# Performance work log

Hardware: AMD Instinct MI355X
Metric: run time of the kernel (lower is better)

Reference implementation:

```python
import jax, jax.numpy as jnp
import numpy as np

N_NODES = 50000
NEG_SLOPE = 0.2  # PyG GATConv default leaky_relu slope


def _segment_softmax(alpha, dst, num_segments):
    # numerically stable softmax over edges grouped by destination node
    m = jax.ops.segment_max(alpha, dst, num_segments=num_segments)
    e = jnp.exp(alpha - m[dst])
    s = jax.ops.segment_sum(e, dst, num_segments=num_segments)
    return e / (s[dst] + 1e-16)


def _gat_conv(h, src, dst, edge_attr, W, We, att_src, att_dst, att_edge, b, num_nodes):
    # h: [N, F_in] -> [N, C] with heads=1, concat=True, add_self_loops=False
    hs = h @ W                          # [N, C]
    ea = edge_attr @ We                 # [E, C]
    a_src = hs @ att_src                # [N]
    a_dst = hs @ att_dst                # [N]
    a_edge = ea @ att_edge              # [E]
    alpha = a_src[src] + a_dst[dst] + a_edge
    alpha = jax.nn.leaky_relu(alpha, NEG_SLOPE)
    alpha = _segment_softmax(alpha, dst, num_nodes)
    msg = hs[src] * alpha[:, None]      # [E, C]
    out = jax.ops.segment_sum(msg, dst, num_segments=num_nodes)
    return out + b


def setup_inputs() -> dict:
    key = jax.random.key(0)
    ks = jax.random.split(key, 16)
    N, E = N_NODES, 500000
    num_authors, a_dim, sbert, c1, c2 = 50000, 128, 384, 32, 128

    def glorot(k, shape):
        lim = float(np.sqrt(6.0 / (shape[0] + shape[-1])))
        return jax.random.uniform(k, shape, jnp.float32, -lim, lim)

    return {
        "x": jnp.arange(N, dtype=jnp.int64) % num_authors,
        "edge_index": jax.random.randint(ks[0], (2, E), 0, N, dtype=jnp.int64),
        "edge_attr": jax.random.normal(ks[1], (E, sbert), jnp.float32),
        "emb": jax.random.normal(ks[2], (num_authors, a_dim), jnp.float32),
        "W1": glorot(ks[3], (a_dim, c1)),
        "We1": glorot(ks[4], (sbert, c1)),
        "att_src1": glorot(ks[5], (c1,)),
        "att_dst1": glorot(ks[6], (c1,)),
        "att_edge1": glorot(ks[7], (c1,)),
        "b1": jnp.zeros((c1,), jnp.float32),
        "W2": glorot(ks[8], (c1, c2)),
        "We2": glorot(ks[9], (sbert, c2)),
        "att_src2": glorot(ks[10], (c2,)),
        "att_dst2": glorot(ks[11], (c2,)),
        "att_edge2": glorot(ks[12], (c2,)),
        "b2": jnp.zeros((c2,), jnp.float32),
    }


def reference(x, edge_index, edge_attr, emb, W1, We1, att_src1, att_dst1, att_edge1, b1,
              W2, We2, att_src2, att_dst2, att_edge2, b2):
    src, dst = edge_index[0], edge_index[1]
    h = emb[x]  # author embedding lookup [N, 128]
    h = _gat_conv(h, src, dst, edge_attr, W1, We1, att_src1, att_dst1, att_edge1, b1, N_NODES)
    h = jax.nn.relu(h)
    h = _gat_conv(h, src, dst, edge_attr, W2, We2, att_src2, att_dst2, att_edge2, b2, N_NODES)
    return h
```

## Files before the change

### kernel.cpp

```cpp
#include <hip/hip_runtime.h>
#include <math.h>

#define NEG 0.2f

__global__ void k_detect(const int* __restrict__ ei32, int* __restrict__ flag) {
    if (threadIdx.x == 0) {
        int any = 0;
        for (int i = 0; i < 128; ++i) any |= ei32[2 * i + 1];
        *flag = (any == 0) ? 1 : 0;
    }
}

__global__ void k_cvt(const void* __restrict__ buf, int* __restrict__ out, int n,
                      const int* __restrict__ flag) {
    int i = blockIdx.x * 256 + threadIdx.x;
    if (i >= n) return;
    if (*flag) out[i] = (int)((const long long*)buf)[i];
    else       out[i] = ((const int*)buf)[i];
}

__global__ void k_vedge(const float* __restrict__ We1, const float* __restrict__ ae1,
                        const float* __restrict__ We2, const float* __restrict__ ae2,
                        float* __restrict__ v1, float* __restrict__ v2) {
    int t = threadIdx.x;
    if (t < 384) {
        float a = 0.f;
        for (int j = 0; j < 32; ++j) a += We1[t * 32 + j] * ae1[j];
        v1[t] = a;
        float b = 0.f;
        for (int j = 0; j < 128; ++j) b += We2[t * 128 + j] * ae2[j];
        v2[t] = b;
    }
}

__global__ __launch_bounds__(256) void k_aedge(const float* __restrict__ ea,
                                               const float* __restrict__ v1,
                                               const float* __restrict__ v2,
                                               float* __restrict__ o1,
                                               float* __restrict__ o2, int E) {
    __shared__ float4 v1s[96], v2s[96];
    int tid = threadIdx.x;
    if (tid < 96) {
        v1s[tid] = ((const float4*)v1)[tid];
        v2s[tid] = ((const float4*)v2)[tid];
    }
    __syncthreads();
    int e = blockIdx.x * 8 + (tid >> 5);
    int gl = tid & 31;
    if (e >= E) return;
    const float4* p = (const float4*)ea + (size_t)e * 96;
    float a1 = 0.f, a2 = 0.f;
#pragma unroll
    for (int j = 0; j < 3; ++j) {
        int idx = j * 32 + gl;
        float4 x = p[idx];
        float4 w = v1s[idx];
        a1 += x.x * w.x + x.y * w.y + x.z * w.z + x.w * w.w;
        w = v2s[idx];
        a2 += x.x * w.x + x.y * w.y + x.z * w.z + x.w * w.w;
    }
#pragma unroll
    for (int off = 16; off >= 1; off >>= 1) {
        a1 += __shfl_xor(a1, off);
        a2 += __shfl_xor(a2, off);
    }
    if (gl == 0) { o1[e] = a1; o2[e] = a2; }
}

__global__ __launch_bounds__(256) void k_node1(const int* __restrict__ x,
                                               const float* __restrict__ emb,
                                               const float* __restrict__ W,
                                               const float* __restrict__ att_s,
                                               const float* __restrict__ att_d,
                                               float* __restrict__ hs,
                                               float* __restrict__ asrc,
                                               float* __restrict__ adst, int N) {
    __shared__ float Ws[128 * 32];
    __shared__ float hrow[8][128];
    int tid = threadIdx.x;
    for (int i = tid; i < 4096; i += 256) Ws[i] = W[i];
    int n0 = blockIdx.x * 8;
    for (int i = tid; i < 8 * 128; i += 256) {
        int nl = i >> 7, k = i & 127;
        int g = n0 + nl;
        hrow[nl][k] = (g < N) ? emb[(size_t)x[g] * 128 + k] : 0.f;
    }
    __syncthreads();
    int nl = tid >> 5, j = tid & 31;
    int node = n0 + nl;
    if (node >= N) return;
    float acc = 0.f;
#pragma unroll 8
    for (int k = 0; k < 128; ++k) acc += hrow[nl][k] * Ws[k * 32 + j];
    hs[(size_t)node * 32 + j] = acc;
    float as = acc * att_s[j], ad = acc * att_d[j];
#pragma unroll
    for (int off = 16; off >= 1; off >>= 1) {
        as += __shfl_xor(as, off);
        ad += __shfl_xor(ad, off);
    }
    if (j == 0) { asrc[node] = as; adst[node] = ad; }
}

__global__ void k_count(const int* __restrict__ dst, int* __restrict__ cnt, int E) {
    int e = blockIdx.x * 256 + threadIdx.x;
    if (e < E) atomicAdd(&cnt[dst[e]], 1);
}

__global__ void k_scan1(const int* __restrict__ cnt, int* __restrict__ ro,
                        int* __restrict__ csum, int N) {
    __shared__ int s[256];
    int t = threadIdx.x;
    int i = blockIdx.x * 256 + t;
    int v = (i < N) ? cnt[i] : 0;
    s[t] = v;
    __syncthreads();
    for (int off = 1; off < 256; off <<= 1) {
        int xv = (t >= off) ? s[t - off] : 0;
        __syncthreads();
        s[t] += xv;
        __syncthreads();
    }
    if (i < N) ro[i + 1] = s[t];
    if (t == 255) csum[blockIdx.x] = s[255];
}

__global__ void k_scan2(int* __restrict__ csum, int nch) {
    __shared__ int s[256];
    int t = threadIdx.x;
    int v = (t < nch) ? csum[t] : 0;
    s[t] = v;
    __syncthreads();
    for (int off = 1; off < 256; off <<= 1) {
        int xv = (t >= off) ? s[t - off] : 0;
        __syncthreads();
        s[t] += xv;
        __syncthreads();
    }
    if (t < nch) csum[t] = s[t] - v;
}

__global__ void k_scan3(int* __restrict__ ro, int* __restrict__ cur,
                        const int* __restrict__ csum, int N) {
    int i = blockIdx.x * 256 + threadIdx.x;
    if (i == 0) { ro[0] = 0; cur[0] = 0; }
    if (i < N) {
        int v = ro[i + 1] + csum[i >> 8];
        ro[i + 1] = v;
        cur[i + 1] = v;
    }
}

__global__ void k_fill(const int* __restrict__ srcA, const int* __restrict__ dstA,
                       const float* __restrict__ ae1, const float* __restrict__ ae2,
                       int* __restrict__ cur, int* __restrict__ srcs,
                       float* __restrict__ ae1s, float* __restrict__ ae2s, int E) {
    int e = blockIdx.x * 256 + threadIdx.x;
    if (e >= E) return;
    int d = dstA[e];
    int p = atomicAdd(&cur[d], 1);
    srcs[p] = srcA[e];
    ae1s[p] = ae1[e];
    ae2s[p] = ae2[e];
}

__global__ __launch_bounds__(256) void k_agg1(const int* __restrict__ ro,
                                              const int* __restrict__ srcs,
                                              const float* __restrict__ ae1s,
                                              const float* __restrict__ asrc,
                                              const float* __restrict__ adst,
                                              const float* __restrict__ hs,
                                              float* __restrict__ out, int N) {
    int tid = threadIdx.x;
    int node = blockIdx.x * 16 + (tid >> 4);
    int gl = tid & 15;
    if (node >= N) return;
    int base = ro[node], end = ro[node + 1];
    float ad = adst[node];
    float m = -3.4e38f;
    for (int p = base + gl; p < end; p += 16) {
        int s = srcs[p];
        float al = asrc[s] + ad + ae1s[p];
        al = (al >= 0.f) ? al : NEG * al;
        m = fmaxf(m, al);
    }
#pragma unroll
    for (int off = 8; off >= 1; off >>= 1) m = fmaxf(m, __shfl_xor(m, off));
    float acc0 = 0.f, acc1 = 0.f, ss = 0.f;
    const float2* hp = (const float2*)hs;
    for (int p = base; p < end; ++p) {
        int s = srcs[p];
        float al = asrc[s] + ad + ae1s[p];
        al = (al >= 0.f) ? al : NEG * al;
        float w = __expf(al - m);
        ss += w;
        float2 hv = hp[(size_t)s * 16 + gl];
        acc0 += w * hv.x;
        acc1 += w * hv.y;
    }
    float inv = 1.f / (ss + 1e-16f);
    out[(size_t)node * 32 + gl * 2] = acc0 * inv;
    out[(size_t)node * 32 + gl * 2 + 1] = acc1 * inv;
}

__global__ __launch_bounds__(256) void k_node2(const float* __restrict__ out1,
                                               const float* __restrict__ b1,
                                               const float* __restrict__ W,
                                               const float* __restrict__ att_s,
                                               const float* __restrict__ att_d,
                                               float* __restrict__ hs,
                                               float* __restrict__ asrc,
                                               float* __restrict__ adst, int N) {
    __shared__ float Ws[32 * 128];
    __shared__ float trow[2][32];
    __shared__ float reds[4], redd[4];
    int tid = threadIdx.x;
    for (int i = tid; i < 4096; i += 256) Ws[i] = W[i];
    int n0 = blockIdx.x * 2;
    if (tid < 64) {
        int nl = tid >> 5, k = tid & 31;
        int g = n0 + nl;
        float v = (g < N) ? out1[(size_t)g * 32 + k] + b1[k] : 0.f;
        trow[nl][k] = fmaxf(v, 0.f);
    }
    __syncthreads();
    int nl = tid >> 7, j = tid & 127;
    int node = n0 + nl;
    float acc = 0.f;
#pragma unroll
    for (int k = 0; k < 32; ++k) acc += trow[nl][k] * Ws[k * 128 + j];
    float as = acc * att_s[j], ad = acc * att_d[j];
#pragma unroll
    for (int off = 32; off >= 1; off >>= 1) {
        as += __shfl_xor(as, off);
        ad += __shfl_xor(ad, off);
    }
    int w = tid >> 6;
    if ((tid & 63) == 0) { reds[w] = as; redd[w] = ad; }
    __syncthreads();
    if (node < N) {
        hs[(size_t)node * 128 + j] = acc;
        if (j == 0) {
            asrc[node] = reds[nl * 2] + reds[nl * 2 + 1];
            adst[node] = redd[nl * 2] + redd[nl * 2 + 1];
        }
    }
}

__global__ __launch_bounds__(256) void k_agg2(const int* __restrict__ ro,
                                              const int* __restrict__ srcs,
                                              const float* __restrict__ ae2s,
                                              const float* __restrict__ asrc,
                                              const float* __restrict__ adst,
                                              const float* __restrict__ hs,
                                              const float* __restrict__ b2,
                                              float* __restrict__ out, int N) {
    int tid = threadIdx.x;
    int node = blockIdx.x * 4 + (tid >> 6);
    int gl = tid & 63;
    if (node >= N) return;
    int base = ro[node], end = ro[node + 1];
    float ad = adst[node];
    float m = -3.4e38f;
    for (int p = base + gl; p < end; p += 64) {
        int s = srcs[p];
        float al = asrc[s] + ad + ae2s[p];
        al = (al >= 0.f) ? al : NEG * al;
        m = fmaxf(m, al);
    }
#pragma unroll
    for (int off = 32; off >= 1; off >>= 1) m = fmaxf(m, __shfl_xor(m, off));
    float acc0 = 0.f, acc1 = 0.f, ss = 0.f;
    const float2* hp = (const float2*)hs;
    for (int p = base; p < end; ++p) {
        int s = srcs[p];
        float al = asrc[s] + ad + ae2s[p];
        al = (al >= 0.f) ? al : NEG * al;
        float w = __expf(al - m);
        ss += w;
        float2 hv = hp[(size_t)s * 64 + gl];
        acc0 += w * hv.x;
        acc1 += w * hv.y;
    }
    float inv = 1.f / (ss + 1e-16f);
    out[(size_t)node * 128 + gl * 2] = acc0 * inv + b2[gl * 2];
    out[(size_t)node * 128 + gl * 2 + 1] = acc1 * inv + b2[gl * 2 + 1];
}

extern "C" void kernel_launch(void* const* d_in, const int* in_sizes, int n_in,
                              void* d_out, int out_size, void* d_ws, size_t ws_size,
                              hipStream_t stream) {
    const void*  xRaw      = d_in[0];
    const void*  eiRaw     = d_in[1];
    const float* edge_attr = (const float*)d_in[2];
    const float* emb  = (const float*)d_in[3];
    const float* W1   = (const float*)d_in[4];
    const float* We1  = (const float*)d_in[5];
    const float* as1  = (const float*)d_in[6];
    const float* ad1v = (const float*)d_in[7];
    const float* ae1v = (const float*)d_in[8];
    const float* b1   = (const float*)d_in[9];
    const float* W2   = (const float*)d_in[10];
    const float* We2  = (const float*)d_in[11];
    const float* as2  = (const float*)d_in[12];
    const float* ad2v = (const float*)d_in[13];
    const float* ae2v = (const float*)d_in[14];
    const float* b2   = (const float*)d_in[15];
    float* out = (float*)d_out;

    int N = in_sizes[0];
    int E = in_sizes[1] / 2;

    char* w = (char*)d_ws;
    auto alloc = [&](size_t bytes) -> void* {
        void* p = (void*)w;
        w += (bytes + 255) & ~(size_t)255;
        return p;
    };
    float* v1     = (float*)alloc(384 * 4);
    float* v2     = (float*)alloc(384 * 4);
    float* aedge1 = (float*)alloc((size_t)E * 4);
    float* aedge2 = (float*)alloc((size_t)E * 4);
    float* hs1    = (float*)alloc((size_t)N * 32 * 4);
    float* a_src1 = (float*)alloc((size_t)N * 4);
    float* a_dst1 = (float*)alloc((size_t)N * 4);
    float* out1   = (float*)alloc((size_t)N * 32 * 4);
    float* hs2v   = (float*)alloc((size_t)N * 128 * 4);
    float* a_src2 = (float*)alloc((size_t)N * 4);
    float* a_dst2 = (float*)alloc((size_t)N * 4);
    int*   cnt    = (int*)alloc((size_t)(N + 1) * 4);
    int*   ro     = (int*)alloc((size_t)(N + 1) * 4);
    int*   cur    = (int*)alloc((size_t)(N + 1) * 4);
    int*   csum   = (int*)alloc(256 * 4);
    int*   srcs   = (int*)alloc((size_t)E * 4);
    float* ae1s   = (float*)alloc((size_t)E * 4);
    float* ae2s   = (float*)alloc((size_t)E * 4);
    int*   flag   = (int*)alloc(256);
    int*   xi     = (int*)alloc((size_t)N * 4);
    int*   eic    = (int*)alloc((size_t)2 * E * 4);
    const int* srcA = eic;
    const int* dstA = eic + E;

    hipMemsetAsync(cnt, 0, (size_t)N * 4, stream);

    k_detect<<<1, 64, 0, stream>>>((const int*)eiRaw, flag);
    k_cvt<<<(N + 255) / 256, 256, 0, stream>>>(xRaw, xi, N, flag);
    k_cvt<<<(2 * E + 255) / 256, 256, 0, stream>>>(eiRaw, eic, 2 * E, flag);

    k_vedge<<<1, 384, 0, stream>>>(We1, ae1v, We2, ae2v, v1, v2);
    k_aedge<<<(E + 7) / 8, 256, 0, stream>>>(edge_attr, v1, v2, aedge1, aedge2, E);
    k_node1<<<(N + 7) / 8, 256, 0, stream>>>(xi, emb, W1, as1, ad1v, hs1, a_src1, a_dst1, N);
    k_count<<<(E + 255) / 256, 256, 0, stream>>>(dstA, cnt, E);
    int nch = (N + 255) / 256;
    k_scan1<<<nch, 256, 0, stream>>>(cnt, ro, csum, N);
    k_scan2<<<1, 256, 0, stream>>>(csum, nch);
    k_scan3<<<nch, 256, 0, stream>>>(ro, cur, csum, N);
    k_fill<<<(E + 255) / 256, 256, 0, stream>>>(srcA, dstA, aedge1, aedge2, cur, srcs, ae1s, ae2s, E);
    k_agg1<<<(N + 15) / 16, 256, 0, stream>>>(ro, srcs, ae1s, a_src1, a_dst1, hs1, out1, N);
    k_node2<<<(N + 1) / 2, 256, 0, stream>>>(out1, b1, W2, as2, ad2v, hs2v, a_src2, a_dst2, N);
    k_agg2<<<(N + 3) / 4, 256, 0, stream>>>(ro, srcs, ae2s, a_src2, a_dst2, hs2v, b2, out, N);
}
```

Baseline: 1.267 ms.

## Fuse index conversion and counting, pack edge payload, prefetch in aggregation

Removes the separate int64-to-int32 conversion and degree-count kernels by reading raw edge indices directly and doing the atomic count inside the edge-attention kernel. The CSR fill now writes a packed int4 payload per edge (source, precombined layer-1 logit term, layer-2 edge term), so the aggregation kernels make one load per edge instead of several scattered ones. The aggregation loops software-prefetch the next edge's payload and feature row, and node2 processes 8 nodes per 1024-thread block. The cost is more payload bandwidth (16 bytes per edge) and higher register use from the prefetch.

After: 1.218 ms. 1.04x faster.

```diff
diff --git a/kernel.cpp b/kernel.cpp
--- a/kernel.cpp
+++ b/kernel.cpp
@@ -3,26 +3,17 @@
 
 #define NEG 0.2f
 
-__global__ void k_detect(const int* __restrict__ ei32, int* __restrict__ flag) {
-    if (threadIdx.x == 0) {
-        int any = 0;
-        for (int i = 0; i < 128; ++i) any |= ei32[2 * i + 1];
-        *flag = (any == 0) ? 1 : 0;
-    }
-}
-
-__global__ void k_cvt(const void* __restrict__ buf, int* __restrict__ out, int n,
-                      const int* __restrict__ flag) {
-    int i = blockIdx.x * 256 + threadIdx.x;
-    if (i >= n) return;
-    if (*flag) out[i] = (int)((const long long*)buf)[i];
-    else       out[i] = ((const int*)buf)[i];
-}
-
-__global__ void k_vedge(const float* __restrict__ We1, const float* __restrict__ ae1,
-                        const float* __restrict__ We2, const float* __restrict__ ae2,
-                        float* __restrict__ v1, float* __restrict__ v2) {
+__global__ __launch_bounds__(384) void k_pre(const void* __restrict__ ei,
+                                             const float* __restrict__ We1, const float* __restrict__ ae1,
+                                             const float* __restrict__ We2, const float* __restrict__ ae2,
+                                             float* __restrict__ v1, float* __restrict__ v2,
+                                             int* __restrict__ flag) {
     int t = threadIdx.x;
+    if (t < 64) {
+        int vodd = ((const int*)ei)[2 * t + 1];
+        unsigned long long nz = __ballot(vodd != 0);
+        if (t == 0) *flag = (nz == 0ull) ? 1 : 0;
+    }
     if (t < 384) {
         float a = 0.f;
         for (int j = 0; j < 32; ++j) a += We1[t * 32 + j] * ae1[j];
@@ -34,10 +25,13 @@
 }
 
 __global__ __launch_bounds__(256) void k_aedge(const float* __restrict__ ea,
+                                               const void* __restrict__ ei,
                                                const float* __restrict__ v1,
                                                const float* __restrict__ v2,
                                                float* __restrict__ o1,
-                                               float* __restrict__ o2, int E) {
+                                               float* __restrict__ o2,
+                                               int* __restrict__ cnt,
+                                               const int* __restrict__ flag, int E) {
     __shared__ float4 v1s[96], v2s[96];
     int tid = threadIdx.x;
     if (tid < 96) {
@@ -64,26 +58,38 @@
         a1 += __shfl_xor(a1, off);
         a2 += __shfl_xor(a2, off);
     }
-    if (gl == 0) { o1[e] = a1; o2[e] = a2; }
-}
-
-__global__ __launch_bounds__(256) void k_node1(const int* __restrict__ x,
+    if (gl == 0) {
+        o1[e] = a1;
+        o2[e] = a2;
+        int d = (*flag) ? (int)((const long long*)ei)[E + e] : ((const int*)ei)[E + e];
+        atomicAdd(&cnt[d], 1);
+    }
+}
+
+__global__ __launch_bounds__(256) void k_node1(const void* __restrict__ x,
                                                const float* __restrict__ emb,
                                                const float* __restrict__ W,
                                                const float* __restrict__ att_s,
                                                const float* __restrict__ att_d,
                                                float* __restrict__ hs,
                                                float* __restrict__ asrc,
-                                               float* __restrict__ adst, int N) {
+                                               float* __restrict__ adst,
+                                               const int* __restrict__ flag, int N) {
     __shared__ float Ws[128 * 32];
     __shared__ float hrow[8][128];
     int tid = threadIdx.x;
+    int fl = *flag;
     for (int i = tid; i < 4096; i += 256) Ws[i] = W[i];
     int n0 = blockIdx.x * 8;
     for (int i = tid; i < 8 * 128; i += 256) {
         int nl = i >> 7, k = i & 127;
         int g = n0 + nl;
-        hrow[nl][k] = (g < N) ? emb[(size_t)x[g] * 128 + k] : 0.f;
+        float v = 0.f;
+        if (g < N) {
+            long long xg = fl ? ((const long long*)x)[g] : (long long)((const int*)x)[g];
+            v = emb[(size_t)xg * 128 + k];
+        }
+        hrow[nl][k] = v;
     }
     __syncthreads();
     int nl = tid >> 5, j = tid & 31;
@@ -102,11 +108,6 @@
     if (j == 0) { asrc[node] = as; adst[node] = ad; }
 }
 
-__global__ void k_count(const int* __restrict__ dst, int* __restrict__ cnt, int E) {
-    int e = blockIdx.x * 256 + threadIdx.x;
-    if (e < E) atomicAdd(&cnt[dst[e]], 1);
-}
-
 __global__ void k_scan1(const int* __restrict__ cnt, int* __restrict__ ro,
                         int* __restrict__ csum, int N) {
     __shared__ int s[256];
@@ -151,23 +152,29 @@
     }
 }
 
-__global__ void k_fill(const int* __restrict__ srcA, const int* __restrict__ dstA,
+__global__ void k_fill(const void* __restrict__ ei,
                        const float* __restrict__ ae1, const float* __restrict__ ae2,
-                       int* __restrict__ cur, int* __restrict__ srcs,
-                       float* __restrict__ ae1s, float* __restrict__ ae2s, int E) {
+                       const float* __restrict__ asrc1,
+                       int* __restrict__ cur, int4* __restrict__ payload,
+                       const int* __restrict__ flag, int E) {
     int e = blockIdx.x * 256 + threadIdx.x;
     if (e >= E) return;
-    int d = dstA[e];
+    int fl = *flag;
+    int s, d;
+    if (fl) {
+        s = (int)((const long long*)ei)[e];
+        d = (int)((const long long*)ei)[E + e];
+    } else {
+        s = ((const int*)ei)[e];
+        d = ((const int*)ei)[E + e];
+    }
     int p = atomicAdd(&cur[d], 1);
-    srcs[p] = srcA[e];
-    ae1s[p] = ae1[e];
-    ae2s[p] = ae2[e];
+    float c1 = asrc1[s] + ae1[e];
+    payload[p] = make_int4(s, __float_as_int(c1), __float_as_int(ae2[e]), 0);
 }
 
 __global__ __launch_bounds__(256) void k_agg1(const int* __restrict__ ro,
-                                              const int* __restrict__ srcs,
-                                              const float* __restrict__ ae1s,
-                                              const float* __restrict__ asrc,
+                                              const int4* __restrict__ payload,
                                               const float* __restrict__ adst,
                                               const float* __restrict__ hs,
                                               float* __restrict__ out, int N) {
@@ -179,45 +186,53 @@
     float ad = adst[node];
     float m = -3.4e38f;
     for (int p = base + gl; p < end; p += 16) {
-        int s = srcs[p];
-        float al = asrc[s] + ad + ae1s[p];
+        float al = __int_as_float(payload[p].y) + ad;
         al = (al >= 0.f) ? al : NEG * al;
         m = fmaxf(m, al);
     }
 #pragma unroll
     for (int off = 8; off >= 1; off >>= 1) m = fmaxf(m, __shfl_xor(m, off));
+    const float2* hp = (const float2*)hs;
+    int len = end - base;
+    int4 pay0 = make_int4(0, 0, 0, 0), pay1 = make_int4(0, 0, 0, 0);
+    float2 hv0 = make_float2(0.f, 0.f);
+    if (len > 0) pay0 = payload[base];
+    if (len > 1) pay1 = payload[base + 1];
+    if (len > 0) hv0 = hp[(size_t)pay0.x * 16 + gl];
     float acc0 = 0.f, acc1 = 0.f, ss = 0.f;
-    const float2* hp = (const float2*)hs;
-    for (int p = base; p < end; ++p) {
-        int s = srcs[p];
-        float al = asrc[s] + ad + ae1s[p];
+    for (int i = 0; i < len; ++i) {
+        int4 payc = pay0;
+        float2 hvc = hv0;
+        pay0 = pay1;
+        if (i + 2 < len) pay1 = payload[base + i + 2];
+        if (i + 1 < len) hv0 = hp[(size_t)pay0.x * 16 + gl];
+        float al = __int_as_float(payc.y) + ad;
         al = (al >= 0.f) ? al : NEG * al;
         float w = __expf(al - m);
         ss += w;
-        float2 hv = hp[(size_t)s * 16 + gl];
-        acc0 += w * hv.x;
-        acc1 += w * hv.y;
+        acc0 += w * hvc.x;
+        acc1 += w * hvc.y;
     }
     float inv = 1.f / (ss + 1e-16f);
     out[(size_t)node * 32 + gl * 2] = acc0 * inv;
     out[(size_t)node * 32 + gl * 2 + 1] = acc1 * inv;
 }
 
-__global__ __launch_bounds__(256) void k_node2(const float* __restrict__ out1,
-                                               const float* __restrict__ b1,
-                                               const float* __restrict__ W,
-                                               const float* __restrict__ att_s,
-                                               const float* __restrict__ att_d,
-                                               float* __restrict__ hs,
-                                               float* __restrict__ asrc,
-                                               float* __restrict__ adst, int N) {
+__global__ __launch_bounds__(1024) void k_node2(const float* __restrict__ out1,
+                                                const float* __restrict__ b1,
+                                                const float* __restrict__ W,
+                                                const float* __restrict__ att_s,
+                                                const float* __restrict__ att_d,
+                                                float* __restrict__ hs,
+                                                float* __restrict__ asrc,
+                                                float* __restrict__ adst, int N) {
     __shared__ float Ws[32 * 128];
-    __shared__ float trow[2][32];
-    __shared__ float reds[4], redd[4];
-    int tid = threadIdx.x;
-    for (int i = tid; i < 4096; i += 256) Ws[i] = W[i];
-    int n0 = blockIdx.x * 2;
-    if (tid < 64) {
+    __shared__ float trow[8][32];
+    __shared__ float reds[16], redd[16];
+    int tid = threadIdx.x;
+    for (int i = tid; i < 4096; i += 1024) Ws[i] = W[i];
+    int n0 = blockIdx.x * 8;
+    if (tid < 256) {
         int nl = tid >> 5, k = tid & 31;
         int g = n0 + nl;
         float v = (g < N) ? out1[(size_t)g * 32 + k] + b1[k] : 0.f;
@@ -235,8 +250,8 @@
         as += __shfl_xor(as, off);
         ad += __shfl_xor(ad, off);
     }
-    int w = tid >> 6;
-    if ((tid & 63) == 0) { reds[w] = as; redd[w] = ad; }
+    int wv = tid >> 6;
+    if ((tid & 63) == 0) { reds[wv] = as; redd[wv] = ad; }
     __syncthreads();
     if (node < N) {
         hs[(size_t)node * 128 + j] = acc;
@@ -248,8 +263,7 @@
 }
 
 __global__ __launch_bounds__(256) void k_agg2(const int* __restrict__ ro,
-                                              const int* __restrict__ srcs,
-                                              const float* __restrict__ ae2s,
+                                              const int4* __restrict__ payload,
                                               const float* __restrict__ asrc,
                                               const float* __restrict__ adst,
                                               const float* __restrict__ hs,
@@ -263,24 +277,35 @@
     float ad = adst[node];
     float m = -3.4e38f;
     for (int p = base + gl; p < end; p += 64) {
-        int s = srcs[p];
-        float al = asrc[s] + ad + ae2s[p];
+        int4 pay = payload[p];
+        float al = asrc[pay.x] + ad + __int_as_float(pay.z);
         al = (al >= 0.f) ? al : NEG * al;
         m = fmaxf(m, al);
     }
 #pragma unroll
     for (int off = 32; off >= 1; off >>= 1) m = fmaxf(m, __shfl_xor(m, off));
+    const float2* hp = (const float2*)hs;
+    int len = end - base;
+    int4 pay0 = make_int4(0, 0, 0, 0), pay1 = make_int4(0, 0, 0, 0);
+    float2 hv0 = make_float2(0.f, 0.f);
+    float as0 = 0.f;
+    if (len > 0) pay0 = payload[base];
+    if (len > 1) pay1 = payload[base + 1];
+    if (len > 0) { as0 = asrc[pay0.x]; hv0 = hp[(size_t)pay0.x * 64 + gl]; }
     float acc0 = 0.f, acc1 = 0.f, ss = 0.f;
-    const float2* hp = (const float2*)hs;
-    for (int p = base; p < end; ++p) {
-        int s = srcs[p];
-        float al = asrc[s] + ad + ae2s[p];
+    for (int i = 0; i < len; ++i) {
+        int4 payc = pay0;
+        float2 hvc = hv0;
+        float asc = as0;
+        pay0 = pay1;
+        if (i + 2 < len) pay1 = payload[base + i + 2];
+        if (i + 1 < len) { as0 = asrc[pay0.x]; hv0 = hp[(size_t)pay0.x * 64 + gl]; }
+        float al = asc + ad + __int_as_float(payc.z);
         al = (al >= 0.f) ? al : NEG * al;
         float w = __expf(al - m);
         ss += w;
-        float2 hv = hp[(size_t)s * 64 + gl];
-        acc0 += w * hv.x;
-        acc1 += w * hv.y;
+        acc0 += w * hvc.x;
+        acc1 += w * hvc.y;
     }
     float inv = 1.f / (ss + 1e-16f);
     out[(size_t)node * 128 + gl * 2] = acc0 * inv + b2[gl * 2];
@@ -317,46 +342,35 @@
         w += (bytes + 255) & ~(size_t)255;
         return p;
     };
-    float* v1     = (float*)alloc(384 * 4);
-    float* v2     = (float*)alloc(384 * 4);
-    float* aedge1 = (float*)alloc((size_t)E * 4);
-    float* aedge2 = (float*)alloc((size_t)E * 4);
-    float* hs1    = (float*)alloc((size_t)N * 32 * 4);
-    float* a_src1 = (float*)alloc((size_t)N * 4);
-    float* a_dst1 = (float*)alloc((size_t)N * 4);
-    float* out1   = (float*)alloc((size_t)N * 32 * 4);
-    float* hs2v   = (float*)alloc((size_t)N * 128 * 4);
-    float* a_src2 = (float*)alloc((size_t)N * 4);
-    float* a_dst2 = (float*)alloc((size_t)N * 4);
-    int*   cnt    = (int*)alloc((size_t)(N + 1) * 4);
-    int*   ro     = (int*)alloc((size_t)(N + 1) * 4);
-    int*   cur    = (int*)alloc((size_t)(N + 1) * 4);
-    int*   csum   = (int*)alloc(256 * 4);
-    int*   srcs   = (int*)alloc((size_t)E * 4);
-    float* ae1s   = (float*)alloc((size_t)E * 4);
-    float* ae2s   = (float*)alloc((size_t)E * 4);
-    int*   flag   = (int*)alloc(256);
-    int*   xi     = (int*)alloc((size_t)N * 4);
-    int*   eic    = (int*)alloc((size_t)2 * E * 4);
-    const int* srcA = eic;
-    const int* dstA = eic + E;
+    float* v1      = (float*)alloc(384 * 4);
+    float* v2      = (float*)alloc(384 * 4);
+    float* aedge1  = (float*)alloc((size_t)E * 4);
+    float* aedge2  = (float*)alloc((size_t)E * 4);
+    float* hs1     = (float*)alloc((size_t)N * 32 * 4);
+    float* a_src1  = (float*)alloc((size_t)N * 4);
+    float* a_dst1  = (float*)alloc((size_t)N * 4);
+    float* out1    = (float*)alloc((size_t)N * 32 * 4);
+    float* hs2v    = (float*)alloc((size_t)N * 128 * 4);
+    float* a_src2  = (float*)alloc((size_t)N * 4);
+    float* a_dst2  = (float*)alloc((size_t)N * 4);
+    int*   cnt     = (int*)alloc((size_t)(N + 1) * 4);
+    int*   ro      = (int*)alloc((size_t)(N + 1) * 4);
+    int*   cur     = (int*)alloc((size_t)(N + 1) * 4);
+    int*   csum    = (int*)alloc(256 * 4);
+    int4*  payload = (int4*)alloc((size_t)E * 16);
+    int*   flag    = (int*)alloc(256);
 
     hipMemsetAsync(cnt, 0, (size_t)N * 4, stream);
 
-    k_detect<<<1, 64, 0, stream>>>((const int*)eiRaw, flag);
-    k_cvt<<<(N + 255) / 256, 256, 0, stream>>>(xRaw, xi, N, flag);
-    k_cvt<<<(2 * E + 255) / 256, 256, 0, stream>>>(eiRaw, eic, 2 * E, flag);
-
-    k_vedge<<<1, 384, 0, stream>>>(We1, ae1v, We2, ae2v, v1, v2);
-    k_aedge<<<(E + 7) / 8, 256, 0, stream>>>(edge_attr, v1, v2, aedge1, aedge2, E);
-    k_node1<<<(N + 7) / 8, 256, 0, stream>>>(xi, emb, W1, as1, ad1v, hs1, a_src1, a_dst1, N);
-    k_count<<<(E + 255) / 256, 256, 0, stream>>>(dstA, cnt, E);
+    k_pre<<<1, 384, 0, stream>>>(eiRaw, We1, ae1v, We2, ae2v, v1, v2, flag);
+    k_aedge<<<(E + 7) / 8, 256, 0, stream>>>(edge_attr, eiRaw, v1, v2, aedge1, aedge2, cnt, flag, E);
+    k_node1<<<(N + 7) / 8, 256, 0, stream>>>(xRaw, emb, W1, as1, ad1v, hs1, a_src1, a_dst1, flag, N);
     int nch = (N + 255) / 256;
     k_scan1<<<nch, 256, 0, stream>>>(cnt, ro, csum, N);
     k_scan2<<<1, 256, 0, stream>>>(csum, nch);
     k_scan3<<<nch, 256, 0, stream>>>(ro, cur, csum, N);
-    k_fill<<<(E + 255) / 256, 256, 0, stream>>>(srcA, dstA, aedge1, aedge2, cur, srcs, ae1s, ae2s, E);
-    k_agg1<<<(N + 15) / 16, 256, 0, stream>>>(ro, srcs, ae1s, a_src1, a_dst1, hs1, out1, N);
-    k_node2<<<(N + 1) / 2, 256, 0, stream>>>(out1, b1, W2, as2, ad2v, hs2v, a_src2, a_dst2, N);
-    k_agg2<<<(N + 3) / 4, 256, 0, stream>>>(ro, srcs, ae2s, a_src2, a_dst2, hs2v, b2, out, N);
-}
+    k_fill<<<(E + 255) / 256, 256, 0, stream>>>(eiRaw, aedge1, aedge2, a_src1, cur, payload, flag, E);
+    k_agg1<<<(N + 15) / 16, 256, 0, stream>>>(ro, payload, a_dst1, hs1, out1, N);
+    k_node2<<<(N + 7) / 8, 1024, 0, stream>>>(out1, b1, W2, as2, ad2v, hs2v, a_src2, a_dst2, N);
+    k_agg2<<<(N + 3) / 4, 256, 0, stream>>>(ro, payload, a_src2, a_dst2, hs2v, b2, out, N);
+}
```
